# Optimization experiments

Hardware: AMD Instinct MI355X
Metric: run time of the kernel (lower is better)

Reference implementation:

```python
import jax, jax.numpy as jnp
import numpy as np

B, C, H, W = 8, 64, 256, 256
N_HEADS = 4
MODES_X, MODES_Y = 32, 32 // 2 + 1  # rfft half-spectrum along last dim
O_PER_HEAD = C // N_HEADS


def setup_inputs() -> dict:
    key = jax.random.key(0)
    k1, k2, k3 = jax.random.split(key, 3)
    x = jax.random.normal(k1, (B, C, H, W), dtype=jnp.float32)
    weights_real = jax.random.normal(k2, (N_HEADS, C, O_PER_HEAD, MODES_X, MODES_Y), dtype=jnp.float32) * 0.01
    weights_imag = jax.random.normal(k3, (N_HEADS, C, O_PER_HEAD, MODES_X, MODES_Y), dtype=jnp.float32) * 0.01
    bias = jnp.zeros((C, 1, 1), dtype=jnp.float32)
    return {"x": x, "weights_real": weights_real, "weights_imag": weights_imag, "bias": bias}


def reference(x, weights_real, weights_imag, bias):
    b, c, h, w = x.shape
    nh, _, o, mxw, myw = weights_real.shape
    # rfft2 with ortho norm, matching torch.fft.rfft2(..., norm='ortho')
    xf = jnp.fft.rfft2(x, norm="ortho")  # [B, C, H, W//2+1] complex64
    fH, fW = xf.shape[-2], xf.shape[-1]
    mx = min(mxw, fH)
    my = min(myw, fW)
    wgt = weights_real[..., :mx, :my] + 1j * weights_imag[..., :mx, :my]  # [nh, C, o, mx, my]
    # all heads at once: torch loop 'biXY,ioXY->boXY' per head == 'bixy,hioxy->bhoxy'
    prod = jnp.einsum("bixy,hioxy->bhoxy", xf[:, :, :mx, :my], wgt)  # [B, nh, o, mx, my]
    out_f = jnp.zeros((b, nh, o, fH, fW), dtype=prod.dtype).at[..., :mx, :my].set(prod)
    out = jnp.fft.irfft2(out_f, s=(h, w), norm="ortho")  # [B, nh, o, H, W] real
    # torch.cat over heads along channel dim == head-major reshape
    out = out.reshape(b, nh * o, h, w)
    return out + bias  # bias [C,1,1] broadcasts
```

## Files before the change

kernel.cpp:

```cpp
#include <hip/hip_runtime.h>
#include <hip/hip_bf16.h>

#define NROWS 131072
#define MY 17
#define MX 32


#define K1_ROWS 30
#define NCHUNK 9
#define PLANE 2044

__global__ __launch_bounds__(512) void f1_fw(const float* __restrict__ x,
                                             float2* __restrict__ X2) {
    __shared__ __align__(16) float s_lds[4 * PLANE];
    __shared__ float2 xs[4352];
    int t = threadIdx.x;
    int bc = blockIdx.x;
    const float* xp = x + (long)bc * 65536;

    int g = t / 9;
    int e = t % 9;
    int odd = (e >= 5);
    int j0 = odd ? 4 * e - 19 : 4 * e;
    int j1 = j0 + 2;
    float ca = odd ? 0.f : 1.f;
    float cb = odd ? -1.f : 0.f;
    float cj0, sj0, cj1, sj1;
    sincospif((float)j0 * (1.0f / 128.0f), &sj0, &cj0); sj0 = -sj0;
    sincospif((float)j1 * (1.0f / 128.0f), &sj1, &cj1); sj1 = -sj1;
    float c80, s80, c81, s81;
    sincospif((float)j0 * 0.25f, &s80, &c80); s80 = -s80;
    sincospif((float)j1 * 0.25f, &s81, &c81); s81 = -s81;
    const float4* A4 = (const float4*)(s_lds + (odd ? PLANE : 0) + g * 68);
    const float4* B4 = (const float4*)(s_lds + (odd ? 3 * PLANE : 2 * PLANE) + g * 68);

    float4 q0, q1, q2, q3;

#define F1_REGLOAD(cc)                                                         \
    {                                                                          \
        int nr_ = ((cc) < 8) ? K1_ROWS : 16;                                   \
        int items_ = nr_ * 16;                                                 \
        int it = t < items_ ? t : items_ - 1;                                  \
        int rr = it >> 4, cq = it & 15;                                        \
        const float4* xr =                                                     \
            (const float4*)(xp + ((cc) * K1_ROWS + rr) * 256) + cq;            \
        q0 = xr[0];                                                            \
        q1 = xr[16];                                                           \
        q2 = xr[32];                                                           \
        q3 = xr[48];                                                           \
    }

    F1_REGLOAD(0)

    for (int c = 0; c < NCHUNK; ++c) {
        int nr = (c < 8) ? K1_ROWS : 16;
        int items = nr * 16;

        if (t < items) {
            int rr = t >> 4, cq = t & 15;
            float4 s02p, s02m, s13p, s13m;
            s02p.x = q0.x + q2.x; s02p.y = q0.y + q2.y;
            s02p.z = q0.z + q2.z; s02p.w = q0.w + q2.w;
            s02m.x = q0.x - q2.x; s02m.y = q0.y - q2.y;
            s02m.z = q0.z - q2.z; s02m.w = q0.w - q2.w;
            s13p.x = q1.x + q3.x; s13p.y = q1.y + q3.y;
            s13p.z = q1.z + q3.z; s13p.w = q1.w + q3.w;
            s13m.x = q1.x - q3.x; s13m.y = q1.y - q3.y;
            s13m.z = q1.z - q3.z; s13m.w = q1.w - q3.w;
            int base = rr * 68 + cq * 4;
            *(float4*)&s_lds[base]             = s02p;
            *(float4*)&s_lds[PLANE + base]     = s02m;
            *(float4*)&s_lds[2 * PLANE + base] = s13p;
            *(float4*)&s_lds[3 * PLANE + base] = s13m;
        }
        __syncthreads();

        if (c + 1 < NCHUNK) F1_REGLOAD(c + 1)

        if (t < 270 && g < nr) {
            float pc0 = 1.f, ps0 = 0.f, pc1 = 1.f, ps1 = 0.f;
            float ar0 = 0, ai0 = 0, ar1 = 0, ai1 = 0;

#define K1_STEP(aL, bL, aH, bH)                                        \
  { float y0Lre = fmaf(ca, (bL), (aL));                                \
    float y0Lim = cb * (bL);                                           \
    float y1Lre = fmaf(-ca, (bL), (aL));                               \
    float y0Hre = fmaf(ca, (bH), (aH));                                \
    float y0Him = cb * (bH);                                           \
    float y1Hre = fmaf(-ca, (bH), (aH));                               \
    float t0re = fmaf(-s80, y0Him, fmaf(c80, y0Hre, y0Lre));           \
    float t0im = fmaf(s80, y0Hre, fmaf(c80, y0Him, y0Lim));            \
    float t1re = fmaf(s81, y0Him, fmaf(c81, y1Hre, y1Lre));            \
    float t1im = fmaf(s81, y1Hre, fmaf(-c81, y0Him, -y0Lim));          \
    ar0 = fmaf(t0re, pc0, ar0); ar0 = fmaf(-t0im, ps0, ar0);           \
    ai0 = fmaf(t0re, ps0, ai0); ai0 = fmaf(t0im, pc0, ai0);            \
    ar1 = fmaf(t1re, pc1, ar1); ar1 = fmaf(-t1im, ps1, ar1);           \
    ai1 = fmaf(t1re, ps1, ai1); ai1 = fmaf(t1im, pc1, ai1);            \
    float nps0 = fmaf(pc0, sj0, ps0 * cj0);                            \
    pc0 = fmaf(pc0, cj0, -(ps0 * sj0)); ps0 = nps0;                    \
    float nps1 = fmaf(pc1, sj1, ps1 * cj1);                            \
    pc1 = fmaf(pc1, cj1, -(ps1 * sj1)); ps1 = nps1; }

#pragma unroll 2
            for (int l4 = 0; l4 < 8; ++l4) {
                float4 va = A4[l4], vb = B4[l4];
                float4 vA = A4[8 + l4], vB = B4[8 + l4];
                K1_STEP(va.x, vb.x, vA.x, vB.x)
                K1_STEP(va.y, vb.y, vA.y, vB.y)
                K1_STEP(va.z, vb.z, vA.z, vB.z)
                K1_STEP(va.w, vb.w, vA.w, vB.w)
            }
#undef K1_STEP

            int h = c * K1_ROWS + g;
            xs[h * 17 + j0] = make_float2(ar0, ai0);
            if (j1 < 17) xs[h * 17 + j1] = make_float2(ar1, ai1);
        }
        __syncthreads();
    }

    for (int q = t; q < 2176; q += 512) {
        float2 a = xs[q], b = xs[q + 2176];
        xs[q] = make_float2(a.x + b.x, a.y + b.y);
        xs[q + 2176] = make_float2(a.x - b.x, a.y - b.y);
    }
    __syncthreads();

    if (t < 272) {
        int grp = t / 17, ky = t % 17;
        int kodd = (grp >= 8);
        int kx0 = kodd ? 4 * (grp - 8) + 1 : 4 * grp;
        int kx1 = kx0 + 2;
        float cA = kodd ? 0.f : 1.f;
        float cB = kodd ? -1.f : 0.f;
        float cs0, ss0, cs1, ss1;
        sincospif((float)kx0 * (1.0f / 128.0f), &ss0, &cs0); ss0 = -ss0;
        sincospif((float)kx1 * (1.0f / 128.0f), &ss1, &cs1); ss1 = -ss1;
        const float2* Aq = xs + (kodd ? 2176 : 0) + ky;
        float pc0 = 1.f, ps0 = 0.f, pc1 = 1.f, ps1 = 0.f;
        float ar0 = 0, ai0 = 0, ar1 = 0, ai1 = 0;
#pragma unroll 4
        for (int m = 0; m < 64; ++m) {
            float2 a = Aq[m * 17];
            float2 b = Aq[1088 + m * 17];
            float yre0 = fmaf(-cB, b.y, fmaf(cA, b.x, a.x));
            float yim0 = fmaf(cB, b.x, fmaf(cA, b.y, a.y));
            float yre1 = fmaf(2.f, a.x, -yre0);
            float yim1 = fmaf(2.f, a.y, -yim0);
            ar0 = fmaf(yre0, pc0, ar0); ar0 = fmaf(-yim0, ps0, ar0);
            ai0 = fmaf(yre0, ps0, ai0); ai0 = fmaf(yim0, pc0, ai0);
            ar1 = fmaf(yre1, pc1, ar1); ar1 = fmaf(-yim1, ps1, ar1);
            ai1 = fmaf(yre1, ps1, ai1); ai1 = fmaf(yim1, pc1, ai1);
            float nps0 = fmaf(pc0, ss0, ps0 * cs0);
            pc0 = fmaf(pc0, cs0, -(ps0 * ss0)); ps0 = nps0;
            float nps1 = fmaf(pc1, ss1, ps1 * cs1);
            pc1 = fmaf(pc1, cs1, -(ps1 * ss1)); ps1 = nps1;
        }
        X2[(long)bc * 544 + kx0 * 17 + ky] = make_float2(ar0, ai0);
        X2[(long)bc * 544 + kx1 * 17 + ky] = make_float2(ar1, ai1);
    }
#undef F1_REGLOAD
}

__global__ __launch_bounds__(512) void f2c_inv(const float2* __restrict__ X2,
                                               const float* __restrict__ wr_g,
                                               const float* __restrict__ wi_g,
                                               const float* __restrict__ bias,
                                               float* __restrict__ out) {
    __shared__ float2 psh[544];
    __shared__ float2 zsh[4352];
    int t = threadIdx.x;
    int plane = blockIdx.x;
    int b = plane >> 6;
    int ho = plane & 63;
    int n = ho >> 4;
    int o = ho & 15;

    for (int q = t; q < 544; q += 512) {
        const float2* xp = X2 + (long)b * 64 * 544 + q;
        const float* wrp = wr_g + ((long)(n * 64) * 16 + o) * 544 + q;
        const float* wip = wi_g + ((long)(n * 64) * 16 + o) * 544 + q;
        float ar = 0.f, ai = 0.f, ar2 = 0.f, ai2 = 0.f;
#pragma unroll 4
        for (int i = 0; i < 64; i += 2) {
            float2 xv0 = xp[i * 544];
            float w0r = wrp[i * 8704];
            float w0i = wip[i * 8704];
            float2 xv1 = xp[(i + 1) * 544];
            float w1r = wrp[(i + 1) * 8704];
            float w1i = wip[(i + 1) * 8704];
            ar = fmaf(xv0.x, w0r, fmaf(-xv0.y, w0i, ar));
            ai = fmaf(xv0.x, w0i, fmaf(xv0.y, w0r, ai));
            ar2 = fmaf(xv1.x, w1r, fmaf(-xv1.y, w1i, ar2));
            ai2 = fmaf(xv1.x, w1i, fmaf(xv1.y, w1r, ai2));
        }
        psh[q] = make_float2(ar + ar2, ai + ai2);
    }
    __syncthreads();

    {
        int h = t & 127;
        int grp = t >> 7;
        int kyb = (grp == 0) ? 0 : (4 * grp + 1);
        int cnt = (grp == 0) ? 5 : 4;
        float chh, shh;
        sincospif((float)h * (1.0f / 128.0f), &shh, &chh);
        float pc = 1.f, psn = 0.f;
        float aer[5], aei[5], aor[5], aoi[5];
#pragma unroll
        for (int u = 0; u < 5; ++u) { aer[u] = 0.f; aei[u] = 0.f; aor[u] = 0.f; aoi[u] = 0.f; }

        const float2* pq = psh + kyb;
#pragma unroll
        for (int kx = 0; kx < 32; ++kx) {
#pragma unroll
            for (int u = 0; u < 5; ++u) {
                if (u < cnt) {
                    float2 v = pq[kx * 17 + u];
                    if ((kx & 1) == 0) {
                        aer[u] = fmaf(v.x, pc, fmaf(-v.y, psn, aer[u]));
                        aei[u] = fmaf(v.x, psn, fmaf(v.y, pc, aei[u]));
                    } else {
                        aor[u] = fmaf(v.x, pc, fmaf(-v.y, psn, aor[u]));
                        aoi[u] = fmaf(v.x, psn, fmaf(v.y, pc, aoi[u]));
                    }
                }
            }
            float npc = pc * chh - psn * shh;
            psn = pc * shh + psn * chh;
            pc = npc;
        }
#pragma unroll
        for (int u = 0; u < 5; ++u) {
            if (u < cnt) {
                int ky = kyb + u;
                zsh[h * 17 + ky] = make_float2(aer[u] + aor[u], aei[u] + aoi[u]);
                zsh[(h + 128) * 17 + ky] = make_float2(aer[u] - aor[u], aei[u] - aoi[u]);
            }
        }
    }
    __syncthreads();

    int wv = t >> 6;
    int lane = t & 63;
    float bv = bias[plane & 63];
    float c0, s0;
    sincospif((float)lane * (1.0f / 128.0f), &s0, &c0);
    float c8, s8;
    sincospif((float)lane * (1.0f / 16.0f), &s8, &c8);

    float pcv[8], psv[8];
    {
        float pc = c0, ps = s0;
#pragma unroll
        for (int k = 0; k < 8; ++k) {
            pcv[k] = pc; psv[k] = ps;
            float nps = fmaf(pc, s0, ps * c0);
            pc = fmaf(pc, c0, -(ps * s0));
            ps = nps;
        }
    }

    const float inv = 1.0f / 65536.0f;
    const float inv2 = 2.0f / 65536.0f;
    long ob_plane = (long)plane * 65536;
    int li = lane < 34 ? lane : 33;

    for (int it16 = 0; it16 < 16; ++it16) {
        int r0 = it16 * 16 + wv * 2;
        float2 zl = zsh[r0 * 17 + li];
        float zlx = zl.x, zly = zl.y;

#define RLF(v, l) __int_as_float(__builtin_amdgcn_readlane(__float_as_int(v), (l)))
        float zz0r[8], zz0i[8], zz1r[8], zz1i[8];
#pragma unroll
        for (int k = 0; k < 8; ++k) {
            float a0r = RLF(zlx, k + 1),  a0i = RLF(zly, k + 1);
            float b0r = RLF(zlx, k + 9),  b0i = RLF(zly, k + 9);
            float a1r = RLF(zlx, 18 + k), a1i = RLF(zly, 18 + k);
            float b1r = RLF(zlx, 26 + k), b1i = RLF(zly, 26 + k);
            zz0r[k] = fmaf(b0r, c8, fmaf(-b0i, s8, a0r));
            zz0i[k] = fmaf(b0r, s8, fmaf(b0i, c8, a0i));
            zz1r[k] = fmaf(b1r, c8, fmaf(-b1i, s8, a1r));
            zz1i[k] = fmaf(b1r, s8, fmaf(b1i, c8, a1i));
        }
        float base0 = RLF(zlx, 0) * inv + bv;
        float base1 = RLF(zlx, 17) * inv + bv;
#undef RLF

        float a00 = 0, a01 = 0, a02 = 0, a03 = 0;
        float a10 = 0, a11 = 0, a12 = 0, a13 = 0;
#pragma unroll
        for (int k = 0; k < 8; ++k) {
            int ky = k + 1;
            float A0 = zz0r[k] * pcv[k] - zz0i[k] * psv[k];
            float B0 = zz0r[k] * psv[k] + zz0i[k] * pcv[k];
            float A1 = zz1r[k] * pcv[k] - zz1i[k] * psv[k];
            float B1 = zz1r[k] * psv[k] + zz1i[k] * pcv[k];
            a00 += A0; a10 += A1;
            a01 += ((ky & 3) == 0) ? A0 : ((ky & 3) == 1) ? -B0 : ((ky & 3) == 2) ? -A0 : B0;
            a11 += ((ky & 3) == 0) ? A1 : ((ky & 3) == 1) ? -B1 : ((ky & 3) == 2) ? -A1 : B1;
            a02 += (ky & 1) ? -A0 : A0;
            a12 += (ky & 1) ? -A1 : A1;
            a03 += ((ky & 3) == 0) ? A0 : ((ky & 3) == 1) ? B0 : ((ky & 3) == 2) ? -A0 : -B0;
            a13 += ((ky & 3) == 0) ? A1 : ((ky & 3) == 1) ? B1 : ((ky & 3) == 2) ? -A1 : -B1;
        }
        long ob0 = ob_plane + (long)r0 * 256;
        long ob1 = ob0 + 256;
        out[ob0 + lane]       = fmaf(a00, inv2, base0);
        out[ob0 + 64 + lane]  = fmaf(a01, inv2, base0);
        out[ob0 + 128 + lane] = fmaf(a02, inv2, base0);
        out[ob0 + 192 + lane] = fmaf(a03, inv2, base0);
        out[ob1 + lane]       = fmaf(a10, inv2, base1);
        out[ob1 + 64 + lane]  = fmaf(a11, inv2, base1);
        out[ob1 + 128 + lane] = fmaf(a12, inv2, base1);
        out[ob1 + 192 + lane] = fmaf(a13, inv2, base1);
    }
}

extern "C" void kernel_launch(void* const* d_in, const int* in_sizes, int n_in,
                              void* d_out, int out_size, void* d_ws, size_t ws_size,
                              hipStream_t stream) {
    const float* x = (const float*)d_in[0];
    const float* wr = (const float*)d_in[1];
    const float* wi = (const float*)d_in[2];
    const float* bias = (const float*)d_in[3];
    float* out = (float*)d_out;
    float* ws = (float*)d_ws;

    float2* X2 = (float2*)(ws + 4456960);

    hipLaunchKernelGGL(f1_fw, dim3(512), dim3(512), 0, stream, x, X2);
    hipLaunchKernelGGL(f2c_inv, dim3(512), dim3(512), 0, stream, X2, wr, wi, bias, out);
}
```

Before: 121.0 us.

## Split forward row-DFT across thread pairs and flatten column-DFT to one output per thread

The row-DFT stage in f1_fw now assigns two threads to each (row, frequency-pair) item. Each thread covers half of the 32-element input range, starting from a pre-rotated twiddle, and the two partial sums are combined with a lane shuffle. Chunk size drops from 30 to 28 rows so 504 of the 512 threads are active instead of 270. The column-DFT stage changes from 272 threads each producing two outputs to up to 512 threads each producing one, which needs a second loop iteration for the remaining 32 outputs. This raises thread utilisation but adds shuffles, an extra chunk iteration with its syncs, and some redundant work.

```diff
diff --git a/kernel.cpp b/kernel.cpp
--- a/kernel.cpp
+++ b/kernel.cpp
@@ -6,20 +6,21 @@
 #define MX 32
 
 
-#define K1_ROWS 30
-#define NCHUNK 9
-#define PLANE 2044
+#define K1_ROWS 28
+#define NCHUNK 10
 
 __global__ __launch_bounds__(512) void f1_fw(const float* __restrict__ x,
                                              float2* __restrict__ X2) {
-    __shared__ __align__(16) float s_lds[4 * PLANE];
+    __shared__ __align__(16) float s_lds[4][K1_ROWS][68];
     __shared__ float2 xs[4352];
     int t = threadIdx.x;
     int bc = blockIdx.x;
     const float* xp = x + (long)bc * 65536;
 
-    int g = t / 9;
-    int e = t % 9;
+    int half = t & 1;
+    int u = t >> 1;
+    int e = u % 9;
+    int g = u / 9;
     int odd = (e >= 5);
     int j0 = odd ? 4 * e - 19 : 4 * e;
     int j1 = j0 + 2;
@@ -31,14 +32,18 @@
     float c80, s80, c81, s81;
     sincospif((float)j0 * 0.25f, &s80, &c80); s80 = -s80;
     sincospif((float)j1 * 0.25f, &s81, &c81); s81 = -s81;
-    const float4* A4 = (const float4*)(s_lds + (odd ? PLANE : 0) + g * 68);
-    const float4* B4 = (const float4*)(s_lds + (odd ? 3 * PLANE : 2 * PLANE) + g * 68);
+    float ip0c, ip0s, ip1c, ip1s;
+    sincospif((float)(j0 * half) * 0.125f, &ip0s, &ip0c); ip0s = -ip0s;
+    sincospif((float)(j1 * half) * 0.125f, &ip1s, &ip1c); ip1s = -ip1s;
+    const float4* A4 = (const float4*)&s_lds[odd ? 1 : 0][g < K1_ROWS ? g : 0][0];
+    const float4* B4 = (const float4*)&s_lds[odd ? 3 : 2][g < K1_ROWS ? g : 0][0];
+    int l4b = half * 4;
 
     float4 q0, q1, q2, q3;
 
 #define F1_REGLOAD(cc)                                                         \
     {                                                                          \
-        int nr_ = ((cc) < 8) ? K1_ROWS : 16;                                   \
+        int nr_ = ((cc) < 9) ? K1_ROWS : 4;                                    \
         int items_ = nr_ * 16;                                                 \
         int it = t < items_ ? t : items_ - 1;                                  \
         int rr = it >> 4, cq = it & 15;                                        \
@@ -53,7 +58,7 @@
     F1_REGLOAD(0)
 
     for (int c = 0; c < NCHUNK; ++c) {
-        int nr = (c < 8) ? K1_ROWS : 16;
+        int nr = (c < 9) ? K1_ROWS : 4;
         int items = nr * 16;
 
         if (t < items) {
@@ -67,18 +72,17 @@
             s13p.z = q1.z + q3.z; s13p.w = q1.w + q3.w;
             s13m.x = q1.x - q3.x; s13m.y = q1.y - q3.y;
             s13m.z = q1.z - q3.z; s13m.w = q1.w - q3.w;
-            int base = rr * 68 + cq * 4;
-            *(float4*)&s_lds[base]             = s02p;
-            *(float4*)&s_lds[PLANE + base]     = s02m;
-            *(float4*)&s_lds[2 * PLANE + base] = s13p;
-            *(float4*)&s_lds[3 * PLANE + base] = s13m;
+            *(float4*)&s_lds[0][rr][cq * 4] = s02p;
+            *(float4*)&s_lds[1][rr][cq * 4] = s02m;
+            *(float4*)&s_lds[2][rr][cq * 4] = s13p;
+            *(float4*)&s_lds[3][rr][cq * 4] = s13m;
         }
         __syncthreads();
 
         if (c + 1 < NCHUNK) F1_REGLOAD(c + 1)
 
-        if (t < 270 && g < nr) {
-            float pc0 = 1.f, ps0 = 0.f, pc1 = 1.f, ps1 = 0.f;
+        {
+            float pc0 = ip0c, ps0 = ip0s, pc1 = ip1c, ps1 = ip1s;
             float ar0 = 0, ai0 = 0, ar1 = 0, ai1 = 0;
 
 #define K1_STEP(aL, bL, aH, bH)                                        \
@@ -101,20 +105,28 @@
     float nps1 = fmaf(pc1, sj1, ps1 * cj1);                            \
     pc1 = fmaf(pc1, cj1, -(ps1 * sj1)); ps1 = nps1; }
 
-#pragma unroll 2
-            for (int l4 = 0; l4 < 8; ++l4) {
-                float4 va = A4[l4], vb = B4[l4];
-                float4 vA = A4[8 + l4], vB = B4[8 + l4];
-                K1_STEP(va.x, vb.x, vA.x, vB.x)
-                K1_STEP(va.y, vb.y, vA.y, vB.y)
-                K1_STEP(va.z, vb.z, vA.z, vB.z)
-                K1_STEP(va.w, vb.w, vA.w, vB.w)
+            bool act = (t < 504) && (g < nr);
+            if (act) {
+#pragma unroll
+                for (int k = 0; k < 4; ++k) {
+                    float4 va = A4[l4b + k], vb = B4[l4b + k];
+                    float4 vA = A4[8 + l4b + k], vB = B4[8 + l4b + k];
+                    K1_STEP(va.x, vb.x, vA.x, vB.x)
+                    K1_STEP(va.y, vb.y, vA.y, vB.y)
+                    K1_STEP(va.z, vb.z, vA.z, vB.z)
+                    K1_STEP(va.w, vb.w, vA.w, vB.w)
+                }
             }
 #undef K1_STEP
-
-            int h = c * K1_ROWS + g;
-            xs[h * 17 + j0] = make_float2(ar0, ai0);
-            if (j1 < 17) xs[h * 17 + j1] = make_float2(ar1, ai1);
+            ar0 += __shfl_xor(ar0, 1);
+            ai0 += __shfl_xor(ai0, 1);
+            ar1 += __shfl_xor(ar1, 1);
+            ai1 += __shfl_xor(ai1, 1);
+            if (act && half == 0) {
+                int h = c * K1_ROWS + g;
+                xs[h * 17 + j0] = make_float2(ar0, ai0);
+                if (j1 < 17) xs[h * 17 + j1] = make_float2(ar1, ai1);
+            }
         }
         __syncthreads();
     }
@@ -126,38 +138,31 @@
     }
     __syncthreads();
 
-    if (t < 272) {
-        int grp = t / 17, ky = t % 17;
-        int kodd = (grp >= 8);
-        int kx0 = kodd ? 4 * (grp - 8) + 1 : 4 * grp;
-        int kx1 = kx0 + 2;
-        float cA = kodd ? 0.f : 1.f;
-        float cB = kodd ? -1.f : 0.f;
-        float cs0, ss0, cs1, ss1;
-        sincospif((float)kx0 * (1.0f / 128.0f), &ss0, &cs0); ss0 = -ss0;
-        sincospif((float)kx1 * (1.0f / 128.0f), &ss1, &cs1); ss1 = -ss1;
+    for (int q = t; q < 544; q += 512) {
+        int kx = q / 17, ky = q % 17;
+        int kodd = kx & 1;
+        float cA = kodd ? 0.f : ((kx & 2) ? -1.f : 1.f);
+        float cB = kodd ? (((kx & 3) == 1) ? -1.f : 1.f) : 0.f;
+        float cBn = -cB;
         const float2* Aq = xs + (kodd ? 2176 : 0) + ky;
-        float pc0 = 1.f, ps0 = 0.f, pc1 = 1.f, ps1 = 0.f;
-        float ar0 = 0, ai0 = 0, ar1 = 0, ai1 = 0;
+        float cs, ss;
+        sincospif((float)kx * (1.0f / 128.0f), &ss, &cs);
+        ss = -ss;
+        float pc = 1.f, psn = 0.f;
+        float ar = 0.f, ai = 0.f;
 #pragma unroll 4
         for (int m = 0; m < 64; ++m) {
             float2 a = Aq[m * 17];
             float2 b = Aq[1088 + m * 17];
-            float yre0 = fmaf(-cB, b.y, fmaf(cA, b.x, a.x));
-            float yim0 = fmaf(cB, b.x, fmaf(cA, b.y, a.y));
-            float yre1 = fmaf(2.f, a.x, -yre0);
-            float yim1 = fmaf(2.f, a.y, -yim0);
-            ar0 = fmaf(yre0, pc0, ar0); ar0 = fmaf(-yim0, ps0, ar0);
-            ai0 = fmaf(yre0, ps0, ai0); ai0 = fmaf(yim0, pc0, ai0);
-            ar1 = fmaf(yre1, pc1, ar1); ar1 = fmaf(-yim1, ps1, ar1);
-            ai1 = fmaf(yre1, ps1, ai1); ai1 = fmaf(yim1, pc1, ai1);
-            float nps0 = fmaf(pc0, ss0, ps0 * cs0);
-            pc0 = fmaf(pc0, cs0, -(ps0 * ss0)); ps0 = nps0;
-            float nps1 = fmaf(pc1, ss1, ps1 * cs1);
-            pc1 = fmaf(pc1, cs1, -(ps1 * ss1)); ps1 = nps1;
-        }
-        X2[(long)bc * 544 + kx0 * 17 + ky] = make_float2(ar0, ai0);
-        X2[(long)bc * 544 + kx1 * 17 + ky] = make_float2(ar1, ai1);
+            float yre = fmaf(cBn, b.y, fmaf(cA, b.x, a.x));
+            float yim = fmaf(cB, b.x, fmaf(cA, b.y, a.y));
+            ar = fmaf(yre, pc, ar); ar = fmaf(-yim, psn, ar);
+            ai = fmaf(yre, psn, ai); ai = fmaf(yim, pc, ai);
+            float npc = pc * cs - psn * ss;
+            psn = pc * ss + psn * cs;
+            pc = npc;
+        }
+        X2[(long)bc * 544 + q] = make_float2(ar, ai);
     }
 #undef F1_REGLOAD
 }
```

After: 112.6 us. 1.07x faster.
